# Kernel tuning notes

Measured on AMD Instinct MI355X. Metric: run time of the kernel, lower is better.

## Reference

```python
import jax, jax.numpy as jnp
import numpy as np

VOXEL_DIM = 16
CELL_DIM = 1.0
AA, A = 21, 14  # 20 amino acids + 'X'; atom14 representation
X_LBL = AA - 1  # label used for unknown residues


def make_voxel():
    v = VOXEL_DIM
    ax = jnp.arange(v, dtype=jnp.float32)
    vx = jnp.broadcast_to((ax - v / 2).reshape(-1, 1, 1), (v, v, v))
    vy = jnp.broadcast_to((ax - v / 4).reshape(1, -1, 1), (v, v, v))
    vz = jnp.broadcast_to((ax - v / 2).reshape(1, 1, -1), (v, v, v))
    return CELL_DIM * jnp.stack([vx, vy, vz], axis=3)  # (Vx,Vy,Vz,3)


def setup_inputs() -> dict:
    key = jax.random.key(0)
    k1, k2, k3, k4 = jax.random.split(key, 4)
    ZN = 1024
    C = 3.0 * jax.random.normal(k1, (ZN, A, 3), dtype=jnp.float32)
    L = jax.random.randint(k2, (ZN,), 0, AA)
    atom_mask = jnp.ones((ZN, A), dtype=jnp.float32)
    charges = 0.5 * jax.random.normal(k3, (AA, A), dtype=jnp.float32)
    return {"C": C, "L": L, "atom_mask": atom_mask, "charges": charges}


def get_backbone(C):
    n, ca, c = C[:, 0, :], C[:, 1, :], C[:, 2, :]
    b1 = ca - n
    b2 = c - ca
    b3 = jnp.cross(b1, b2)
    cb = ca - 0.58273431 * b2 + 0.56802827 * b1 - 0.54067466 * b3
    return jnp.stack([n, ca, c, cb], axis=1)  # (ZN,4,3)


def compute_frames(Cb):
    y = Cb[:, 3, :] - Cb[:, 1, :]
    y_unit = y / jnp.clip(jnp.linalg.norm(y, axis=1, keepdims=True), 1e-6)
    x_raw = Cb[:, 2, :] - Cb[:, 0, :]
    x_proj = jnp.sum(x_raw * y_unit, axis=1, keepdims=True)
    x = x_raw - x_proj
    x_unit = x / jnp.clip(jnp.linalg.norm(x, axis=1, keepdims=True), 1e-6)
    z = jnp.cross(x_unit, y_unit)
    z_unit = z / jnp.clip(jnp.linalg.norm(z, axis=1, keepdims=True), 1e-6)
    frames = jnp.stack([x_unit, y_unit, z_unit], axis=1)  # (ZN,3,3)
    return Cb[:, 3, :], frames


def compute_voxels(origins, frames, voxel):
    # rotation[n,x,y,z,s] = sum_u frames[n,u,s] * voxel[x,y,z,u]
    rot = jnp.einsum('nus,xyzu->nxyzs', frames, voxel)
    return origins[:, None, None, None, :] + rot  # (ZN,Vx,Vy,Vz,3)


def compute_fields(C, L, voxels, atom_mask, charges):
    L = jnp.where(L == -1, X_LBL, L)
    # (ZN,Vx,Vy,Vz,A,3)
    dv = voxels[:, :, :, :, None, :] - C[:, None, None, None, :, :]
    d = jnp.linalg.norm(dv, axis=-1, keepdims=True)
    dist_term = dv / (jnp.where(d == 0, 1.0, d) * jnp.clip(d, CELL_DIM) ** 2)
    pc = charges[L] * atom_mask  # (ZN,A)
    fields = jnp.einsum('na,nxyzas->nxyzs', pc, dist_term)
    fn = jnp.linalg.norm(fields, axis=-1, keepdims=True)
    fields = fields / jnp.where(fn == 0, 1.0, fn)
    return jnp.transpose(fields, (0, 4, 1, 2, 3))  # (ZN,3,Vx,Vy,Vz)


def compute_divergence(fields):
    r = CELL_DIM
    fx, fy, fz = fields[:, 0], fields[:, 1], fields[:, 2]
    dx = jnp.concatenate([
        ((fx[:, 1] - fx[:, 0]) / r)[:, None],
        (fx[:, 2:] - fx[:, :-2]) / (2 * r),
        ((fx[:, -1] - fx[:, -2]) / r)[:, None]], axis=1)
    dy = jnp.concatenate([
        ((fy[:, :, 1] - fy[:, :, 0]) / r)[:, :, None],
        (fy[:, :, 2:] - fy[:, :, :-2]) / (2 * r),
        ((fy[:, :, -1] - fy[:, :, -2]) / r)[:, :, None]], axis=2)
    dz = jnp.concatenate([
        ((fz[:, :, :, 1] - fz[:, :, :, 0]) / r)[:, :, :, None],
        (fz[:, :, :, 2:] - fz[:, :, :, :-2]) / (2 * r),
        ((fz[:, :, :, -1] - fz[:, :, :, -2]) / r)[:, :, :, None]], axis=3)
    return (dx + dy + dz)[:, None]  # (ZN,1,Vx,Vy,Vz)


def reference(C, L, atom_mask, charges):
    voxel = make_voxel()
    Cb = get_backbone(C)
    origins, frames = compute_frames(Cb)
    voxels = compute_voxels(origins, frames, voxel)
    fields = compute_fields(C, L, voxels, atom_mask, charges)
    div = compute_divergence(fields)
    return (Cb, div, frames)
```

## Files before the change

kernel.cpp:

```cpp
#include <hip/hip_runtime.h>

#define AA_NUM 21
#define A_NUM  14
#define NPTS   4096
#define BLK    256

__device__ __forceinline__ float rfl(float x) {
    return __int_as_float(__builtin_amdgcn_readfirstlane(__float_as_int(x)));
}

__global__ __launch_bounds__(BLK) void preproc_kernel(
    const float* __restrict__ Cin,
    const int*   __restrict__ Lin,
    const float* __restrict__ Min,
    const float* __restrict__ Qin,
    float*       __restrict__ out,
    int ZN)
{
    __shared__ float s_atom[A_NUM][3];
    __shared__ float s_pc[A_NUM];
    __shared__ float s_fr[12];
    __shared__ float s_fx[8][BLK];
    __shared__ float s_fy[8][BLK];
    __shared__ float s_fz[9][BLK];

    const int n    = blockIdx.x >> 1;
    const int half = blockIdx.x & 1;
    const int zlo  = half << 3;
    const int zmin = half ? 7 : 0;
    const int off  = half;
    const int t = threadIdx.x;
    const size_t div_off = (size_t)ZN * 12;
    const size_t fr_off  = div_off + (size_t)ZN * NPTS;

    if (t < A_NUM) {
        int la = Lin[n];
        la = (la == -1) ? (AA_NUM - 1) : la;
        s_pc[t] = Qin[la * A_NUM + t] * Min[n * A_NUM + t];
        s_atom[t][0] = Cin[(n * A_NUM + t) * 3 + 0];
        s_atom[t][1] = Cin[(n * A_NUM + t) * 3 + 1];
        s_atom[t][2] = Cin[(n * A_NUM + t) * 3 + 2];
    }
    __syncthreads();

    if (t == 0) {
        const float c0 = 0.58273431f, c1 = 0.56802827f, c2 = 0.54067466f;
        float n0x = s_atom[0][0], n0y = s_atom[0][1], n0z = s_atom[0][2];
        float cax = s_atom[1][0], cay = s_atom[1][1], caz = s_atom[1][2];
        float ccx = s_atom[2][0], ccy = s_atom[2][1], ccz = s_atom[2][2];
        float b1x = cax - n0x, b1y = cay - n0y, b1z = caz - n0z;
        float b2x = ccx - cax, b2y = ccy - cay, b2z = ccz - caz;
        float b3x = b1y * b2z - b1z * b2y;
        float b3y = b1z * b2x - b1x * b2z;
        float b3z = b1x * b2y - b1y * b2x;
        float cbx = cax - c0 * b2x + c1 * b1x - c2 * b3x;
        float cby = cay - c0 * b2y + c1 * b1y - c2 * b3y;
        float cbz = caz - c0 * b2z + c1 * b1z - c2 * b3z;

        float yx = cbx - cax, yy = cby - cay, yz = cbz - caz;
        float yr = 1.0f / fmaxf(sqrtf(yx * yx + yy * yy + yz * yz), 1e-6f);
        float yux = yx * yr, yuy = yy * yr, yuz = yz * yr;
        float xrx = ccx - n0x, xry = ccy - n0y, xrz = ccz - n0z;
        float xp = xrx * yux + xry * yuy + xrz * yuz;
        float xx = xrx - xp, xy = xry - xp, xz = xrz - xp;
        float xr = 1.0f / fmaxf(sqrtf(xx * xx + xy * xy + xz * xz), 1e-6f);
        float xux = xx * xr, xuy = xy * xr, xuz = xz * xr;
        float zx = xuy * yuz - xuz * yuy;
        float zy = xuz * yux - xux * yuz;
        float zz = xux * yuy - xuy * yux;
        float zr = 1.0f / fmaxf(sqrtf(zx * zx + zy * zy + zz * zz), 1e-6f);
        float zux = zx * zr, zuy = zy * zr, zuz = zz * zr;

        if (half == 0) {
            float* po = out + (size_t)n * 12;
            po[0]  = n0x; po[1]  = n0y; po[2]  = n0z;
            po[3]  = cax; po[4]  = cay; po[5]  = caz;
            po[6]  = ccx; po[7]  = ccy; po[8]  = ccz;
            po[9]  = cbx; po[10] = cby; po[11] = cbz;
            float* pf = out + fr_off + (size_t)n * 9;
            pf[0] = xux; pf[1] = xuy; pf[2] = xuz;
            pf[3] = yux; pf[4] = yuy; pf[5] = yuz;
            pf[6] = zux; pf[7] = zuy; pf[8] = zuz;
        }

        s_fr[0] = xux; s_fr[1] = xuy; s_fr[2]  = xuz;
        s_fr[3] = yux; s_fr[4] = yuy; s_fr[5]  = yuz;
        s_fr[6] = zux; s_fr[7] = zuy; s_fr[8]  = zuz;
        s_fr[9] = cbx; s_fr[10] = cby; s_fr[11] = cbz;
    }
    __syncthreads();

    float ax[A_NUM], ay[A_NUM], az[A_NUM], aq[A_NUM];
    #pragma unroll
    for (int a = 0; a < A_NUM; ++a) {
        ax[a] = rfl(s_atom[a][0]);
        ay[a] = rfl(s_atom[a][1]);
        az[a] = rfl(s_atom[a][2]);
        aq[a] = rfl(s_pc[a]);
    }
    float fr[12];
    #pragma unroll
    for (int i = 0; i < 12; ++i) fr[i] = rfl(s_fr[i]);

    const int xi = t >> 4;
    const int yi = t & 15;
    const float vx = (float)xi - 8.0f;
    const float vy = (float)yi - 4.0f;
    const float bpx = fr[9]  + vx * fr[0] + vy * fr[3];
    const float bpy = fr[10] + vx * fr[1] + vy * fr[4];
    const float bpz = fr[11] + vx * fr[2] + vy * fr[5];

    for (int l = 0; l < 9; ++l) {
        float vz = (float)(zmin + l) - 8.0f;
        float px = fmaf(vz, fr[6], bpx);
        float py = fmaf(vz, fr[7], bpy);
        float pz = fmaf(vz, fr[8], bpz);
        float fx = 0.0f, fy = 0.0f, fz = 0.0f;
        #pragma unroll
        for (int a = 0; a < A_NUM; ++a) {
            float dx = px - ax[a], dy = py - ay[a], dz = pz - az[a];
            float d2 = dx * dx + dy * dy + dz * dz;
            float rq = __builtin_amdgcn_rsqf(d2);
            float mn = fminf(rq, 1.0f);
            float inv = rq * mn * mn;
            float w = (d2 != 0.0f) ? aq[a] * inv : 0.0f;
            fx = fmaf(w, dx, fx);
            fy = fmaf(w, dy, fy);
            fz = fmaf(w, dz, fz);
        }
        float fn2 = fx * fx + fy * fy + fz * fz;
        float rf = (fn2 != 0.0f) ? __builtin_amdgcn_rsqf(fn2) : 1.0f;
        s_fz[l][t] = fz * rf;
        int li = l - off;
        if (li >= 0 && li < 8) {
            s_fx[li][t] = fx * rf;
            s_fy[li][t] = fy * rf;
        }
    }
    __syncthreads();

    const int cxp = t + ((xi < 15) ? 16 : 0);
    const int cxm = t - ((xi > 0)  ? 16 : 0);
    const int cyp = t + ((yi < 15) ? 1  : 0);
    const int cym = t - ((yi > 0)  ? 1  : 0);
    const float sx = (xi > 0 && xi < 15) ? 0.5f : 1.0f;
    const float sy = (yi > 0 && yi < 15) ? 0.5f : 1.0f;

    float dv[8];
    #pragma unroll
    for (int i = 0; i < 8; ++i) {
        int z = zlo + i;
        int l = i + off;
        int lzp = l + (z < 15);
        int lzm = l - (z > 0);
        float sz = (z > 0 && z < 15) ? 0.5f : 1.0f;
        float dxv = (s_fx[i][cxp] - s_fx[i][cxm]) * sx;
        float dyv = (s_fy[i][cyp] - s_fy[i][cym]) * sy;
        float dzv = (s_fz[lzp][t] - s_fz[lzm][t]) * sz;
        dv[i] = dxv + dyv + dzv;
    }

    float4* dout = (float4*)(out + div_off + (size_t)n * NPTS + t * 16 + zlo);
    dout[0] = make_float4(dv[0], dv[1], dv[2], dv[3]);
    dout[1] = make_float4(dv[4], dv[5], dv[6], dv[7]);
}

extern "C" void kernel_launch(void* const* d_in, const int* in_sizes, int n_in,
                              void* d_out, int out_size, void* d_ws, size_t ws_size,
                              hipStream_t stream) {
    const float* C = (const float*)d_in[0];
    const int*   L = (const int*)d_in[1];
    const float* M = (const float*)d_in[2];
    const float* Q = (const float*)d_in[3];
    float* out = (float*)d_out;
    const int ZN = in_sizes[1];
    preproc_kernel<<<dim3(2 * ZN), dim3(BLK), 0, stream>>>(C, L, M, Q, out, ZN);
}
```

Baseline: 97.34 us.

## Split frame computation into prepass kernel and keep z-field in registers

Moves backbone/frame computation into a separate per-residue kernel that writes atoms, charges and frames into a workspace blob. The field kernel then loads that blob with a single sync instead of a serial thread-0 frame computation between two barriers. The z-component of the field stays in registers with precomputed z-derivatives, which drops the s_fz shared array and raises the occupancy hint. This adds a second kernel launch and a workspace round trip through global memory.

```diff
diff --git a/kernel.cpp b/kernel.cpp
--- a/kernel.cpp
+++ b/kernel.cpp
@@ -4,103 +4,111 @@
 #define A_NUM  14
 #define NPTS   4096
 #define BLK    256
+#define WSTRIDE 80
 
 __device__ __forceinline__ float rfl(float x) {
     return __int_as_float(__builtin_amdgcn_readfirstlane(__float_as_int(x)));
 }
 
-__global__ __launch_bounds__(BLK) void preproc_kernel(
+__global__ void frames_kernel(
     const float* __restrict__ Cin,
     const int*   __restrict__ Lin,
     const float* __restrict__ Min,
     const float* __restrict__ Qin,
     float*       __restrict__ out,
+    float*       __restrict__ ws,
     int ZN)
 {
-    __shared__ float s_atom[A_NUM][3];
-    __shared__ float s_pc[A_NUM];
-    __shared__ float s_fr[12];
+    const int n = blockIdx.x * blockDim.x + threadIdx.x;
+    if (n >= ZN) return;
+    const size_t div_off = (size_t)ZN * 12;
+    const size_t fr_off  = div_off + (size_t)ZN * NPTS;
+
+    const float* c = Cin + (size_t)n * A_NUM * 3;
+    const float c0 = 0.58273431f, c1 = 0.56802827f, c2 = 0.54067466f;
+    float n0x = c[0], n0y = c[1], n0z = c[2];
+    float cax = c[3], cay = c[4], caz = c[5];
+    float ccx = c[6], ccy = c[7], ccz = c[8];
+    float b1x = cax - n0x, b1y = cay - n0y, b1z = caz - n0z;
+    float b2x = ccx - cax, b2y = ccy - cay, b2z = ccz - caz;
+    float b3x = b1y * b2z - b1z * b2y;
+    float b3y = b1z * b2x - b1x * b2z;
+    float b3z = b1x * b2y - b1y * b2x;
+    float cbx = cax - c0 * b2x + c1 * b1x - c2 * b3x;
+    float cby = cay - c0 * b2y + c1 * b1y - c2 * b3y;
+    float cbz = caz - c0 * b2z + c1 * b1z - c2 * b3z;
+
+    float yx = cbx - cax, yy = cby - cay, yz = cbz - caz;
+    float yr = 1.0f / fmaxf(sqrtf(yx * yx + yy * yy + yz * yz), 1e-6f);
+    float yux = yx * yr, yuy = yy * yr, yuz = yz * yr;
+    float xrx = ccx - n0x, xry = ccy - n0y, xrz = ccz - n0z;
+    float xp = xrx * yux + xry * yuy + xrz * yuz;
+    float xx = xrx - xp, xy = xry - xp, xz = xrz - xp;
+    float xr = 1.0f / fmaxf(sqrtf(xx * xx + xy * xy + xz * xz), 1e-6f);
+    float xux = xx * xr, xuy = xy * xr, xuz = xz * xr;
+    float zx = xuy * yuz - xuz * yuy;
+    float zy = xuz * yux - xux * yuz;
+    float zz = xux * yuy - xuy * yux;
+    float zr = 1.0f / fmaxf(sqrtf(zx * zx + zy * zy + zz * zz), 1e-6f);
+    float zux = zx * zr, zuy = zy * zr, zuz = zz * zr;
+
+    float* po = out + (size_t)n * 12;
+    po[0]  = n0x; po[1]  = n0y; po[2]  = n0z;
+    po[3]  = cax; po[4]  = cay; po[5]  = caz;
+    po[6]  = ccx; po[7]  = ccy; po[8]  = ccz;
+    po[9]  = cbx; po[10] = cby; po[11] = cbz;
+    float* pf = out + fr_off + (size_t)n * 9;
+    pf[0] = xux; pf[1] = xuy; pf[2] = xuz;
+    pf[3] = yux; pf[4] = yuy; pf[5] = yuz;
+    pf[6] = zux; pf[7] = zuy; pf[8] = zuz;
+
+    float* blob = ws + (size_t)n * WSTRIDE;
+    int la = Lin[n];
+    la = (la == -1) ? (AA_NUM - 1) : la;
+    #pragma unroll
+    for (int a = 0; a < A_NUM; ++a) {
+        blob[a]          = c[a * 3 + 0];
+        blob[A_NUM + a]  = c[a * 3 + 1];
+        blob[2*A_NUM + a]= c[a * 3 + 2];
+        blob[3*A_NUM + a]= Qin[la * A_NUM + a] * Min[n * A_NUM + a];
+    }
+    blob[56] = xux; blob[57] = xuy; blob[58] = xuz;
+    blob[59] = yux; blob[60] = yuy; blob[61] = yuz;
+    blob[62] = zux; blob[63] = zuy; blob[64] = zuz;
+    blob[65] = cbx; blob[66] = cby; blob[67] = cbz;
+}
+
+__global__ __launch_bounds__(BLK, 8) void field_kernel(
+    const float* __restrict__ ws,
+    float*       __restrict__ out,
+    int ZN)
+{
+    __shared__ float s_blob[68];
     __shared__ float s_fx[8][BLK];
     __shared__ float s_fy[8][BLK];
-    __shared__ float s_fz[9][BLK];
 
     const int n    = blockIdx.x >> 1;
     const int half = blockIdx.x & 1;
-    const int zlo  = half << 3;
     const int zmin = half ? 7 : 0;
     const int off  = half;
+    const int zlo  = half << 3;
     const int t = threadIdx.x;
     const size_t div_off = (size_t)ZN * 12;
-    const size_t fr_off  = div_off + (size_t)ZN * NPTS;
-
-    if (t < A_NUM) {
-        int la = Lin[n];
-        la = (la == -1) ? (AA_NUM - 1) : la;
-        s_pc[t] = Qin[la * A_NUM + t] * Min[n * A_NUM + t];
-        s_atom[t][0] = Cin[(n * A_NUM + t) * 3 + 0];
-        s_atom[t][1] = Cin[(n * A_NUM + t) * 3 + 1];
-        s_atom[t][2] = Cin[(n * A_NUM + t) * 3 + 2];
-    }
+
+    if (t < 68) s_blob[t] = ws[(size_t)n * WSTRIDE + t];
     __syncthreads();
 
-    if (t == 0) {
-        const float c0 = 0.58273431f, c1 = 0.56802827f, c2 = 0.54067466f;
-        float n0x = s_atom[0][0], n0y = s_atom[0][1], n0z = s_atom[0][2];
-        float cax = s_atom[1][0], cay = s_atom[1][1], caz = s_atom[1][2];
-        float ccx = s_atom[2][0], ccy = s_atom[2][1], ccz = s_atom[2][2];
-        float b1x = cax - n0x, b1y = cay - n0y, b1z = caz - n0z;
-        float b2x = ccx - cax, b2y = ccy - cay, b2z = ccz - caz;
-        float b3x = b1y * b2z - b1z * b2y;
-        float b3y = b1z * b2x - b1x * b2z;
-        float b3z = b1x * b2y - b1y * b2x;
-        float cbx = cax - c0 * b2x + c1 * b1x - c2 * b3x;
-        float cby = cay - c0 * b2y + c1 * b1y - c2 * b3y;
-        float cbz = caz - c0 * b2z + c1 * b1z - c2 * b3z;
-
-        float yx = cbx - cax, yy = cby - cay, yz = cbz - caz;
-        float yr = 1.0f / fmaxf(sqrtf(yx * yx + yy * yy + yz * yz), 1e-6f);
-        float yux = yx * yr, yuy = yy * yr, yuz = yz * yr;
-        float xrx = ccx - n0x, xry = ccy - n0y, xrz = ccz - n0z;
-        float xp = xrx * yux + xry * yuy + xrz * yuz;
-        float xx = xrx - xp, xy = xry - xp, xz = xrz - xp;
-        float xr = 1.0f / fmaxf(sqrtf(xx * xx + xy * xy + xz * xz), 1e-6f);
-        float xux = xx * xr, xuy = xy * xr, xuz = xz * xr;
-        float zx = xuy * yuz - xuz * yuy;
-        float zy = xuz * yux - xux * yuz;
-        float zz = xux * yuy - xuy * yux;
-        float zr = 1.0f / fmaxf(sqrtf(zx * zx + zy * zy + zz * zz), 1e-6f);
-        float zux = zx * zr, zuy = zy * zr, zuz = zz * zr;
-
-        if (half == 0) {
-            float* po = out + (size_t)n * 12;
-            po[0]  = n0x; po[1]  = n0y; po[2]  = n0z;
-            po[3]  = cax; po[4]  = cay; po[5]  = caz;
-            po[6]  = ccx; po[7]  = ccy; po[8]  = ccz;
-            po[9]  = cbx; po[10] = cby; po[11] = cbz;
-            float* pf = out + fr_off + (size_t)n * 9;
-            pf[0] = xux; pf[1] = xuy; pf[2] = xuz;
-            pf[3] = yux; pf[4] = yuy; pf[5] = yuz;
-            pf[6] = zux; pf[7] = zuy; pf[8] = zuz;
-        }
-
-        s_fr[0] = xux; s_fr[1] = xuy; s_fr[2]  = xuz;
-        s_fr[3] = yux; s_fr[4] = yuy; s_fr[5]  = yuz;
-        s_fr[6] = zux; s_fr[7] = zuy; s_fr[8]  = zuz;
-        s_fr[9] = cbx; s_fr[10] = cby; s_fr[11] = cbz;
-    }
-    __syncthreads();
-
     float ax[A_NUM], ay[A_NUM], az[A_NUM], aq[A_NUM];
     #pragma unroll
     for (int a = 0; a < A_NUM; ++a) {
-        ax[a] = rfl(s_atom[a][0]);
-        ay[a] = rfl(s_atom[a][1]);
-        az[a] = rfl(s_atom[a][2]);
-        aq[a] = rfl(s_pc[a]);
+        ax[a] = rfl(s_blob[a]);
+        ay[a] = rfl(s_blob[A_NUM + a]);
+        az[a] = rfl(s_blob[2*A_NUM + a]);
+        aq[a] = rfl(s_blob[3*A_NUM + a]);
     }
     float fr[12];
     #pragma unroll
-    for (int i = 0; i < 12; ++i) fr[i] = rfl(s_fr[i]);
+    for (int i = 0; i < 12; ++i) fr[i] = rfl(s_blob[56 + i]);
 
     const int xi = t >> 4;
     const int yi = t & 15;
@@ -109,9 +117,13 @@
     const float bpx = fr[9]  + vx * fr[0] + vy * fr[3];
     const float bpy = fr[10] + vx * fr[1] + vy * fr[4];
     const float bpz = fr[11] + vx * fr[2] + vy * fr[5];
-
+    const float vzbase = (float)zmin - 8.0f;
+
+    float fzv[9];
+
+    #pragma unroll
     for (int l = 0; l < 9; ++l) {
-        float vz = (float)(zmin + l) - 8.0f;
+        float vz = vzbase + (float)l;
         float px = fmaf(vz, fr[6], bpx);
         float py = fmaf(vz, fr[7], bpy);
         float pz = fmaf(vz, fr[8], bpz);
@@ -130,7 +142,7 @@
         }
         float fn2 = fx * fx + fy * fy + fz * fz;
         float rf = (fn2 != 0.0f) ? __builtin_amdgcn_rsqf(fn2) : 1.0f;
-        s_fz[l][t] = fz * rf;
+        fzv[l] = fz * rf;
         int li = l - off;
         if (li >= 0 && li < 8) {
             s_fx[li][t] = fx * rf;
@@ -146,18 +158,27 @@
     const float sx = (xi > 0 && xi < 15) ? 0.5f : 1.0f;
     const float sy = (yi > 0 && yi < 15) ? 0.5f : 1.0f;
 
+    float dzt[8];
+    if (half == 0) {
+        #pragma unroll
+        for (int i = 0; i < 8; ++i) {
+            float sz = (i > 0) ? 0.5f : 1.0f;
+            dzt[i] = (fzv[i + 1] - fzv[(i > 0) ? i - 1 : 0]) * sz;
+        }
+    } else {
+        #pragma unroll
+        for (int i = 0; i < 8; ++i) {
+            float sz = (i < 7) ? 0.5f : 1.0f;
+            dzt[i] = (fzv[(i < 7) ? i + 2 : 8] - fzv[i]) * sz;
+        }
+    }
+
     float dv[8];
     #pragma unroll
     for (int i = 0; i < 8; ++i) {
-        int z = zlo + i;
-        int l = i + off;
-        int lzp = l + (z < 15);
-        int lzm = l - (z > 0);
-        float sz = (z > 0 && z < 15) ? 0.5f : 1.0f;
         float dxv = (s_fx[i][cxp] - s_fx[i][cxm]) * sx;
         float dyv = (s_fy[i][cyp] - s_fy[i][cym]) * sy;
-        float dzv = (s_fz[lzp][t] - s_fz[lzm][t]) * sz;
-        dv[i] = dxv + dyv + dzv;
+        dv[i] = dxv + dyv + dzt[i];
     }
 
     float4* dout = (float4*)(out + div_off + (size_t)n * NPTS + t * 16 + zlo);
@@ -173,6 +194,9 @@
     const float* M = (const float*)d_in[2];
     const float* Q = (const float*)d_in[3];
     float* out = (float*)d_out;
+    float* ws  = (float*)d_ws;
     const int ZN = in_sizes[1];
-    preproc_kernel<<<dim3(2 * ZN), dim3(BLK), 0, stream>>>(C, L, M, Q, out, ZN);
-}
+
+    frames_kernel<<<dim3((ZN + BLK - 1) / BLK), dim3(BLK), 0, stream>>>(C, L, M, Q, out, ws, ZN);
+    field_kernel<<<dim3(2 * ZN), dim3(BLK), 0, stream>>>(ws, out, ZN);
+}
```

New measurement: 111.0 us. 14.1% more time.
